# Kernel tuning notes

Measured on AMD Instinct MI355X. Metric: run time of the kernel, lower is better.

Reference implementation:

```python
import jax, jax.numpy as jnp
import numpy as np

B, DIM, H, W = 8, 256, 128, 128
HEADS, D = 8, 32  # num_heads, qkv_dim (key_dim); multi_q_dim = HEADS*D = DIM


def setup_inputs() -> dict:
    key = jax.random.key(0)
    ks = jax.random.split(key, 10)
    def affine(k, n):
        k1, k2 = jax.random.split(k)
        return (1.0 + 0.1 * jax.random.normal(k1, (n,), jnp.float32),
                0.1 * jax.random.normal(k2, (n,), jnp.float32))
    q_scale, q_bias = affine(ks[1], HEADS * D)
    kv_scale, kv_bias = affine(ks[3], D)
    p_scale, p_bias = affine(ks[5], DIM)
    return {
        "input_": jax.random.normal(ks[0], (B, DIM, H, W), jnp.float32),
        "wq": jax.random.normal(ks[6], (HEADS * D, DIM), jnp.float32) / np.sqrt(DIM),
        "q_scale": q_scale, "q_bias": q_bias,
        "wkv": jax.random.normal(ks[7], (D, DIM), jnp.float32) / np.sqrt(DIM),
        "kv_scale": kv_scale, "kv_bias": kv_bias,
        "wp": jax.random.normal(ks[8], (DIM, HEADS * D), jnp.float32) / np.sqrt(HEADS * D),
        "p_scale": p_scale, "p_bias": p_bias,
    }


def conv1x1_bn(x_flat, w, scale, bias):
    # x_flat: [B,C,N]; 1x1 conv (no bias) fused with eval-mode BN affine
    y = jnp.einsum('oc,bcn->bon', w, x_flat)
    return y * scale[:, None] + bias[:, None]


def reference(input_, wq, q_scale, q_bias, wkv, kv_scale, kv_bias, wp, p_scale, p_bias):
    b, c, h, w = input_.shape
    n = h * w
    xf = input_.reshape(b, c, n)
    # queries: [B, heads, D, N]
    q = conv1x1_bn(xf, wq, q_scale, q_bias).reshape(b, HEADS, D, n)
    # shared key/value, one kv head: [B, D, N]
    kv = conv1x1_bn(xf, wkv, kv_scale, kv_bias)
    key_sm = jax.nn.softmax(kv, axis=2)      # softmax over spatial N
    query_sm = jax.nn.softmax(q, axis=2)     # softmax over channel D
    # context = softmax(K) @ V^T : [B, D, D]
    context = jnp.einsum('bdn,ben->bde', key_sm, kv)
    # attended = context^T @ Q (context broadcast over heads): [B, heads, D, N]
    attended = jnp.einsum('bde,bhdn->bhen', context, query_sm)
    av = attended.reshape(b, HEADS * D, n)
    out = conv1x1_bn(jax.nn.relu(av), wp, p_scale, p_bias)
    return out.reshape(b, c, h, w)
```

## Files before the change

### kernel.cpp

```cpp
#include <hip/hip_runtime.h>
#include <hip/hip_bf16.h>

typedef __attribute__((ext_vector_type(8))) short bf16x8;
typedef __attribute__((ext_vector_type(4))) float f32x4;

#define NB 8
#define NC 256
#define ND 32
#define NN 16384
#define TILE_P 32

#define MFMA16(a, b, c) __builtin_amdgcn_mfma_f32_16x16x32_bf16((a), (b), (c), 0, 0, 0)

__device__ __forceinline__ float u2f(unsigned short u) {
  union { unsigned int i; float f; } v; v.i = ((unsigned int)u) << 16; return v.f;
}
__device__ __forceinline__ unsigned short f2u(float f) {
  union { float f; unsigned int i; } v; v.f = f;
  unsigned int x = v.i;
  return (unsigned short)((x + 0x7fffu + ((x >> 16) & 1u)) >> 16);
}
__device__ __forceinline__ float ldg(const void* p, size_t i, int isbf) {
  return isbf ? u2f(((const unsigned short*)p)[i]) : ((const float*)p)[i];
}
__device__ __forceinline__ char* lds_at(char* base, int p, int colb) {
  return base + (p << 9) + (colb ^ ((p & 7) << 4));
}

__global__ __launch_bounds__(256) void detect_kernel(const void* __restrict__ x,
                                                     int* __restrict__ flag) {
  __shared__ int red[4];
  const unsigned int* w = (const unsigned int*)x;
  int cnt = 0;
  for (int i = threadIdx.x; i < 4096; i += 256) {
    unsigned int e = (w[i] >> 7) & 0xFFu;
    cnt += (e >= 100u && e <= 135u) ? 1 : 0;
  }
  for (int off = 32; off; off >>= 1) cnt += __shfl_xor(cnt, off, 64);
  if ((threadIdx.x & 63) == 0) red[threadIdx.x >> 6] = cnt;
  __syncthreads();
  if (threadIdx.x == 0)
    flag[0] = (red[0] + red[1] + red[2] + red[3] > 2048) ? 1 : 0;
}

__global__ __launch_bounds__(256) void prep_weights(
    const void* __restrict__ wq, const void* __restrict__ wp,
    const void* __restrict__ wkv, const int* __restrict__ flag,
    unsigned short* __restrict__ WqPh, unsigned short* __restrict__ WqPl,
    unsigned short* __restrict__ WpPh, unsigned short* __restrict__ WpPl,
    unsigned short* __restrict__ WkPh, unsigned short* __restrict__ WkPl) {
  int isbf = flag[0];
  int idx = blockIdx.x * 256 + threadIdx.x;
  const void* w;
  unsigned short *Ph, *Pl;
  int slot, o, k0;
  if (idx < 16384) {
    int mat = idx >> 13;
    slot = idx & 8191;
    int lane = slot & 63;
    int mbkt = slot >> 6;
    int mb = mbkt & 15, kt = mbkt >> 4;
    o = mb * 16 + (lane & 15);
    k0 = kt * 32 + (lane >> 4) * 8;
    w = mat ? wp : wq;
    Ph = mat ? WpPh : WqPh;
    Pl = mat ? WpPl : WqPl;
  } else {
    slot = idx - 16384;
    int lane = slot & 63;
    int grp = slot >> 6;
    int mb = grp & 1, kt = grp >> 1;
    o = mb * 16 + (lane & 15);
    k0 = kt * 32 + (lane >> 4) * 8;
    w = wkv;
    Ph = WkPh;
    Pl = WkPl;
  }
  unsigned short h[8], lo[8];
#pragma unroll
  for (int e = 0; e < 8; e++) {
    float v = ldg(w, (size_t)o * NC + k0 + e, isbf);
    unsigned short hh = f2u(v);
    h[e] = hh;
    lo[e] = isbf ? (unsigned short)0 : f2u(v - u2f(hh));
  }
  uint4 ph, pl;
  ph.x = h[0] | ((unsigned)h[1] << 16);
  ph.y = h[2] | ((unsigned)h[3] << 16);
  ph.z = h[4] | ((unsigned)h[5] << 16);
  ph.w = h[6] | ((unsigned)h[7] << 16);
  pl.x = lo[0] | ((unsigned)lo[1] << 16);
  pl.y = lo[2] | ((unsigned)lo[3] << 16);
  pl.z = lo[4] | ((unsigned)lo[5] << 16);
  pl.w = lo[6] | ((unsigned)lo[7] << 16);
  *(uint4*)(Ph + (size_t)slot * 8) = ph;
  *(uint4*)(Pl + (size_t)slot * 8) = pl;
}

__global__ __launch_bounds__(256, 4) void kv_ctx(
    const void* __restrict__ x, const unsigned short* __restrict__ WkPh,
    const unsigned short* __restrict__ WkPl, const void* __restrict__ kv_scale,
    const void* __restrict__ kv_bias, const int* __restrict__ flag,
    float* __restrict__ Spart, float* __restrict__ Zpart) {
  __shared__ __align__(16) char pool[32768];
  const int isbf = flag[0];
  const int tid = threadIdx.x;
  const int bid = blockIdx.x;
  const int b = bid >> 9;
  const int n0 = (bid & 511) * 32;
  const int w = tid >> 6, l = tid & 63, g = l >> 4, cc = l & 15;
  const int mi = w >> 1, ni = w & 1;
  const f32x4 zero4 = {0.f, 0.f, 0.f, 0.f};

  {
    const int c0 = (tid >> 3) * 8;
    const int pq = (tid & 7) * 4;
    unsigned short hi[8][4], lo[8][4];
    if (isbf) {
      const unsigned short* xp =
          (const unsigned short*)x + ((size_t)(b * NC + c0)) * NN + n0 + pq;
#pragma unroll
      for (int i = 0; i < 8; i++) {
        ushort4 r = *(const ushort4*)(xp + (size_t)i * NN);
        hi[i][0] = r.x; hi[i][1] = r.y; hi[i][2] = r.z; hi[i][3] = r.w;
      }
    } else {
      const float* xp = (const float*)x + ((size_t)(b * NC + c0)) * NN + n0 + pq;
#pragma unroll
      for (int i = 0; i < 8; i++) {
        float4 v = *(const float4*)(xp + (size_t)i * NN);
        float vv[4] = {v.x, v.y, v.z, v.w};
#pragma unroll
        for (int j = 0; j < 4; j++) {
          unsigned short hh = f2u(vv[j]);
          hi[i][j] = hh;
          lo[i][j] = f2u(vv[j] - u2f(hh));
        }
      }
    }
#pragma unroll
    for (int j = 0; j < 4; j++) {
      int p = pq + j;
      uint4 wv;
      wv.x = hi[0][j] | ((unsigned)hi[1][j] << 16);
      wv.y = hi[2][j] | ((unsigned)hi[3][j] << 16);
      wv.z = hi[4][j] | ((unsigned)hi[5][j] << 16);
      wv.w = hi[6][j] | ((unsigned)hi[7][j] << 16);
      *(uint4*)lds_at(pool, p, c0 * 2) = wv;
      if (!isbf) {
        uint4 wl2;
        wl2.x = lo[0][j] | ((unsigned)lo[1][j] << 16);
        wl2.y = lo[2][j] | ((unsigned)lo[3][j] << 16);
        wl2.z = lo[4][j] | ((unsigned)lo[5][j] << 16);
        wl2.w = lo[6][j] | ((unsigned)lo[7][j] << 16);
        *(uint4*)lds_at(pool + 16384, p, c0 * 2) = wl2;
      }
    }
  }
  __syncthreads();

  f32x4 acc = zero4;
  {
    const bf16x8* Ah = (const bf16x8*)WkPh;
    const bf16x8* Al = (const bf16x8*)WkPl;
#pragma unroll
    for (int kt = 0; kt < 8; kt++) {
      bf16x8 xb = *(const bf16x8*)lds_at(pool, ni * 16 + cc, kt * 64 + 16 * g);
      bf16x8 a = Ah[(kt * 2 + mi) * 64 + l];
      acc = MFMA16(a, xb, acc);
      if (!isbf) {
        bf16x8 xl = *(const bf16x8*)lds_at(pool + 16384, ni * 16 + cc, kt * 64 + 16 * g);
        bf16x8 al = Al[(kt * 2 + mi) * 64 + l];
        acc = MFMA16(a, xl, acc);
        acc = MFMA16(al, xb, acc);
      }
    }
  }

  unsigned short khv[4], klv[4], ehv[4], elv[4];
  float zv[4];
#pragma unroll
  for (int rr = 0; rr < 4; rr++) {
    int d = mi * 16 + 4 * g + rr;
    float v = acc[rr] * ldg(kv_scale, d, isbf) + ldg(kv_bias, d, isbf);
    unsigned short kh = f2u(v);
    khv[rr] = kh;
    klv[rr] = f2u(v - u2f(kh));
    float e = __expf(v);
    zv[rr] = e;
    unsigned short eh = f2u(e);
    ehv[rr] = eh;
    elv[rr] = f2u(e - u2f(eh));
  }
#pragma unroll
  for (int rr = 0; rr < 4; rr++) {
    zv[rr] += __shfl_xor(zv[rr], 1, 64);
    zv[rr] += __shfl_xor(zv[rr], 2, 64);
    zv[rr] += __shfl_xor(zv[rr], 4, 64);
    zv[rr] += __shfl_xor(zv[rr], 8, 64);
  }
  if (cc == 0) {
#pragma unroll
    for (int rr = 0; rr < 4; rr++)
      Zpart[((size_t)bid * 2 + ni) * ND + mi * 16 + 4 * g + rr] = zv[rr];
  }
  __syncthreads();

  {
    char* Eh = pool;
    char* El = pool + 2048;
    char* Kh = pool + 4096;
    char* Kl = pool + 6144;
    int px = ni * 16 + cc;
#pragma unroll
    for (int rr = 0; rr < 4; rr++) {
      int d = mi * 16 + 4 * g + rr;
      int off = d * 64 + ((px * 2) ^ ((d & 3) << 4));
      *(unsigned short*)(Eh + off) = ehv[rr];
      *(unsigned short*)(El + off) = elv[rr];
      *(unsigned short*)(Kh + off) = khv[rr];
      *(unsigned short*)(Kl + off) = klv[rr];
    }
  }
  __syncthreads();

  {
    char* Eh = pool;
    char* El = pool + 2048;
    char* Kh = pool + 4096;
    char* Kl = pool + 6144;
    int ra = mi * 16 + cc;
    int rb = ni * 16 + cc;
    int ca = (16 * g) ^ ((ra & 3) << 4);
    int cb = (16 * g) ^ ((rb & 3) << 4);
    bf16x8 aEh = *(const bf16x8*)(Eh + ra * 64 + ca);
    bf16x8 aEl = *(const bf16x8*)(El + ra * 64 + ca);
    bf16x8 bKh = *(const bf16x8*)(Kh + rb * 64 + cb);
    bf16x8 bKl = *(const bf16x8*)(Kl + rb * 64 + cb);
    f32x4 s = zero4;
    s = MFMA16(aEh, bKh, s);
    s = MFMA16(aEh, bKl, s);
    s = MFMA16(aEl, bKh, s);
    float* sp = Spart + (size_t)bid * 1024;
#pragma unroll
    for (int rr = 0; rr < 4; rr++)
      sp[(mi * 16 + 4 * g + rr) * 32 + ni * 16 + cc] = s[rr];
  }
}

__global__ __launch_bounds__(256) void ctx_redfin(const float* __restrict__ Spart,
                                                  const float* __restrict__ Zpart,
                                                  float* __restrict__ ctx) {
  __shared__ float rs[256], rz[256];
  const int bid = blockIdx.x;
  const int b = bid >> 5, d = bid & 31;
  const int t = threadIdx.x, e = t & 31, j = t >> 5;
  float s = 0.f;
  for (int c = j; c < 512; c += 8)
    s += Spart[((size_t)(b * 512 + c)) * 1024 + d * 32 + e];
  float z = 0.f;
  for (int k = t; k < 1024; k += 256)
    z += Zpart[((size_t)(b * 1024 + k)) * ND + d];
  rs[t] = s; rz[t] = z;
  __syncthreads();
  if (t < 128) { rs[t] += rs[t + 128]; rz[t] += rz[t + 128]; }
  __syncthreads();
  if (t < 64) { rs[t] += rs[t + 64]; rz[t] += rz[t + 64]; }
  __syncthreads();
  if (t < 32) {
    float ss = rs[t] + rs[t + 32];
    float zz = rz[t] + rz[t + 32];
    zz += __shfl_xor(zz, 1, 64);
    zz += __shfl_xor(zz, 2, 64);
    zz += __shfl_xor(zz, 4, 64);
    zz += __shfl_xor(zz, 8, 64);
    zz += __shfl_xor(zz, 16, 64);
    ctx[((size_t)b * ND + d) * ND + t] = ss / zz;
  }
}

#define XT_OFF 0
#define XTL_OFF 16384
#define SMH_OFF 32768
#define SML_OFF 49152
#define YTH_OFF 0
#define YTL_OFF 16384
#define OT_OFF 32768

__global__ __launch_bounds__(256, 2) void fused_main(
    const void* __restrict__ x,
    const unsigned short* __restrict__ WqPh, const unsigned short* __restrict__ WqPl,
    const unsigned short* __restrict__ WpPh, const unsigned short* __restrict__ WpPl,
    const void* __restrict__ q_scale, const void* __restrict__ q_bias,
    const void* __restrict__ p_scale, const void* __restrict__ p_bias,
    const float* __restrict__ ctx, const int* __restrict__ flag,
    void* __restrict__ out) {
  __shared__ __align__(16) char pool[69632];
  __shared__ float qs_l[NC], qb_l[NC], ps_l[NC], pb_l[NC];
  const int isbf = flag[0];
  const int tid = threadIdx.x;
  const int b = blockIdx.x >> 9;
  const int n0 = (blockIdx.x & 511) * TILE_P;
  const int w = tid >> 6;
  const int l = tid & 63;
  const int g = l >> 4;
  const int cc = l & 15;
  const f32x4 zero4 = {0.f, 0.f, 0.f, 0.f};

  qs_l[tid] = ldg(q_scale, tid, isbf);
  qb_l[tid] = ldg(q_bias, tid, isbf);
  ps_l[tid] = ldg(p_scale, tid, isbf);
  pb_l[tid] = ldg(p_bias, tid, isbf);

  bf16x8 cAh[2], cAl[2];
  {
    const float* cb = ctx + (size_t)b * ND * ND;
#pragma unroll
    for (int mp = 0; mp < 2; mp++) {
      bf16x8 ah, al;
#pragma unroll
      for (int el = 0; el < 8; el++) {
        float v = cb[(8 * g + el) * ND + 16 * mp + cc];
        unsigned short hh = f2u(v);
        ah[el] = (short)hh;
        al[el] = (short)f2u(v - u2f(hh));
      }
      cAh[mp] = ah; cAl[mp] = al;
    }
  }

  {
    const int c0 = (tid >> 3) * 8;
    const int pq = (tid & 7) * 4;
    unsigned short hi[8][4], lo[8][4];
    if (isbf) {
      const unsigned short* xp =
          (const unsigned short*)x + ((size_t)(b * NC + c0)) * NN + n0 + pq;
#pragma unroll
      for (int i = 0; i < 8; i++) {
        ushort4 r = *(const ushort4*)(xp + (size_t)i * NN);
        hi[i][0] = r.x; hi[i][1] = r.y; hi[i][2] = r.z; hi[i][3] = r.w;
      }
    } else {
      const float* xp = (const float*)x + ((size_t)(b * NC + c0)) * NN + n0 + pq;
#pragma unroll
      for (int i = 0; i < 8; i++) {
        float4 v = *(const float4*)(xp + (size_t)i * NN);
        float vv[4] = {v.x, v.y, v.z, v.w};
#pragma unroll
        for (int j = 0; j < 4; j++) {
          unsigned short hh = f2u(vv[j]);
          hi[i][j] = hh;
          lo[i][j] = f2u(vv[j] - u2f(hh));
        }
      }
    }
#pragma unroll
    for (int j = 0; j < 4; j++) {
      int p = pq + j;
      uint4 wv;
      wv.x = hi[0][j] | ((unsigned)hi[1][j] << 16);
      wv.y = hi[2][j] | ((unsigned)hi[3][j] << 16);
      wv.z = hi[4][j] | ((unsigned)hi[5][j] << 16);
      wv.w = hi[6][j] | ((unsigned)hi[7][j] << 16);
      *(uint4*)lds_at(pool + XT_OFF, p, c0 * 2) = wv;
      if (!isbf) {
        uint4 wl2;
        wl2.x = lo[0][j] | ((unsigned)lo[1][j] << 16);
        wl2.y = lo[2][j] | ((unsigned)lo[3][j] << 16);
        wl2.z = lo[4][j] | ((unsigned)lo[5][j] << 16);
        wl2.w = lo[6][j] | ((unsigned)lo[7][j] << 16);
        *(uint4*)lds_at(pool + XTL_OFF, p, c0 * 2) = wl2;
      }
    }
  }
  __syncthreads();

  f32x4 acc[4][2];
#pragma unroll
  for (int mi = 0; mi < 4; mi++) { acc[mi][0] = zero4; acc[mi][1] = zero4; }
  {
    const bf16x8* Aq = (const bf16x8*)WqPh;
    const bf16x8* Aql = (const bf16x8*)WqPl;
#pragma unroll
    for (int kt = 0; kt < 8; kt++) {
      bf16x8 xb0 = *(const bf16x8*)lds_at(pool + XT_OFF, cc, kt * 64 + 16 * g);
      bf16x8 xb1 = *(const bf16x8*)lds_at(pool + XT_OFF, 16 + cc, kt * 64 + 16 * g);
      bf16x8 av[4];
#pragma unroll
      for (int mi = 0; mi < 4; mi++) av[mi] = Aq[(kt * 16 + w * 4 + mi) * 64 + l];
#pragma unroll
      for (int mi = 0; mi < 4; mi++) {
        acc[mi][0] = MFMA16(av[mi], xb0, acc[mi][0]);
        acc[mi][1] = MFMA16(av[mi], xb1, acc[mi][1]);
      }
      if (!isbf) {
        bf16x8 xl0 = *(const bf16x8*)lds_at(pool + XTL_OFF, cc, kt * 64 + 16 * g);
        bf16x8 xl1 = *(const bf16x8*)lds_at(pool + XTL_OFF, 16 + cc, kt * 64 + 16 * g);
#pragma unroll
        for (int mi = 0; mi < 4; mi++) {
          bf16x8 al2 = Aql[(kt * 16 + w * 4 + mi) * 64 + l];
          acc[mi][0] = MFMA16(av[mi], xl0, acc[mi][0]);
          acc[mi][1] = MFMA16(av[mi], xl1, acc[mi][1]);
          acc[mi][0] = MFMA16(al2, xb0, acc[mi][0]);
          acc[mi][1] = MFMA16(al2, xb1, acc[mi][1]);
        }
      }
    }
  }

  float inv_s[2][2];
#pragma unroll
  for (int hp = 0; hp < 2; hp++) {
#pragma unroll
    for (int ni = 0; ni < 2; ni++) {
      float e8[8];
      float mx = -3.0e38f;
#pragma unroll
      for (int mi2 = 0; mi2 < 2; mi2++) {
#pragma unroll
        for (int r = 0; r < 4; r++) {
          int o = w * 64 + (2 * hp + mi2) * 16 + 4 * g + r;
          float v = acc[2 * hp + mi2][ni][r] * qs_l[o] + qb_l[o];
          e8[mi2 * 4 + r] = v;
          mx = fmaxf(mx, v);
        }
      }
      mx = fmaxf(mx, __shfl_xor(mx, 16, 64));
      mx = fmaxf(mx, __shfl_xor(mx, 32, 64));
      float s = 0.f;
#pragma unroll
      for (int i2 = 0; i2 < 8; i2++) { e8[i2] = __expf(e8[i2] - mx); s += e8[i2]; }
      s += __shfl_xor(s, 16, 64);
      s += __shfl_xor(s, 32, 64);
      inv_s[hp][ni] = 1.f / s;
      int p = ni * 16 + cc;
#pragma unroll
      for (int mi2 = 0; mi2 < 2; mi2++) {
        int colb = (w * 64 + (2 * hp + mi2) * 16 + 4 * g) * 2;
        unsigned short h[4], lo2[4];
#pragma unroll
        for (int r = 0; r < 4; r++) {
          float ev = e8[mi2 * 4 + r];
          unsigned short hh = f2u(ev);
          h[r] = hh;
          lo2[r] = f2u(ev - u2f(hh));
        }
        uint2 wh, wl2;
        wh.x = h[0] | ((unsigned)h[1] << 16);
        wh.y = h[2] | ((unsigned)h[3] << 16);
        wl2.x = lo2[0] | ((unsigned)lo2[1] << 16);
        wl2.y = lo2[2] | ((unsigned)lo2[3] << 16);
        *(uint2*)lds_at(pool + SMH_OFF, p, colb) = wh;
        *(uint2*)lds_at(pool + SML_OFF, p, colb) = wl2;
      }
    }
  }
  __syncthreads();

#pragma unroll
  for (int hp = 0; hp < 2; hp++) {
    f32x4 cacc[2][2];
#pragma unroll
    for (int mp = 0; mp < 2; mp++) { cacc[mp][0] = zero4; cacc[mp][1] = zero4; }
#pragma unroll
    for (int ni = 0; ni < 2; ni++) {
      int p = ni * 16 + cc;
      int colb = ((2 * w + hp) * 32 + 8 * g) * 2;
      bf16x8 bh = *(const bf16x8*)lds_at(pool + SMH_OFF, p, colb);
      bf16x8 bl = *(const bf16x8*)lds_at(pool + SML_OFF, p, colb);
#pragma unroll
      for (int mp = 0; mp < 2; mp++) {
        cacc[mp][ni] = MFMA16(cAh[mp], bh, cacc[mp][ni]);
        cacc[mp][ni] = MFMA16(cAh[mp], bl, cacc[mp][ni]);
        cacc[mp][ni] = MFMA16(cAl[mp], bh, cacc[mp][ni]);
      }
    }
#pragma unroll
    for (int mp = 0; mp < 2; mp++) {
#pragma unroll
      for (int ni = 0; ni < 2; ni++) {
        int p = ni * 16 + cc;
        float iv = inv_s[hp][ni];
        unsigned short h[4], lo2[4];
#pragma unroll
        for (int r = 0; r < 4; r++) {
          float y = fmaxf(cacc[mp][ni][r] * iv, 0.f);
          unsigned short hh = f2u(y);
          h[r] = hh;
          lo2[r] = f2u(y - u2f(hh));
        }
        int colb = ((2 * w + hp) * 32 + mp * 16 + 4 * g) * 2;
        uint2 wh, wl2;
        wh.x = h[0] | ((unsigned)h[1] << 16);
        wh.y = h[2] | ((unsigned)h[3] << 16);
        wl2.x = lo2[0] | ((unsigned)lo2[1] << 16);
        wl2.y = lo2[2] | ((unsigned)lo2[3] << 16);
        *(uint2*)lds_at(pool + YTH_OFF, p, colb) = wh;
        *(uint2*)lds_at(pool + YTL_OFF, p, colb) = wl2;
      }
    }
  }
  __syncthreads();

  f32x4 oacc[4][2];
#pragma unroll
  for (int mi = 0; mi < 4; mi++) { oacc[mi][0] = zero4; oacc[mi][1] = zero4; }
  {
    const bf16x8* Ap = (const bf16x8*)WpPh;
    const bf16x8* Apl = (const bf16x8*)WpPl;
#pragma unroll
    for (int kt = 0; kt < 8; kt++) {
      bf16x8 yh0 = *(const bf16x8*)lds_at(pool + YTH_OFF, cc, kt * 64 + 16 * g);
      bf16x8 yh1 = *(const bf16x8*)lds_at(pool + YTH_OFF, 16 + cc, kt * 64 + 16 * g);
      bf16x8 yl0 = *(const bf16x8*)lds_at(pool + YTL_OFF, cc, kt * 64 + 16 * g);
      bf16x8 yl1 = *(const bf16x8*)lds_at(pool + YTL_OFF, 16 + cc, kt * 64 + 16 * g);
      bf16x8 av[4];
#pragma unroll
      for (int mi = 0; mi < 4; mi++) av[mi] = Ap[(kt * 16 + w * 4 + mi) * 64 + l];
#pragma unroll
      for (int mi = 0; mi < 4; mi++) {
        oacc[mi][0] = MFMA16(av[mi], yh0, oacc[mi][0]);
        oacc[mi][1] = MFMA16(av[mi], yh1, oacc[mi][1]);
        oacc[mi][0] = MFMA16(av[mi], yl0, oacc[mi][0]);
        oacc[mi][1] = MFMA16(av[mi], yl1, oacc[mi][1]);
      }
      if (!isbf) {
#pragma unroll
        for (int mi = 0; mi < 4; mi++) {
          bf16x8 al2 = Apl[(kt * 16 + w * 4 + mi) * 64 + l];
          oacc[mi][0] = MFMA16(al2, yh0, oacc[mi][0]);
          oacc[mi][1] = MFMA16(al2, yh1, oacc[mi][1]);
        }
      }
    }
  }

  {
    char* OT = pool + OT_OFF;
#pragma unroll
    for (int mi = 0; mi < 4; mi++) {
#pragma unroll
      for (int ni = 0; ni < 2; ni++) {
#pragma unroll
        for (int r = 0; r < 4; r++) {
          int o = w * 64 + mi * 16 + 4 * g + r;
          float v = oacc[mi][ni][r] * ps_l[o] + pb_l[o];
          int p = ni * 16 + cc;
          if (isbf)
            *(unsigned short*)(OT + o * 80 + p * 2) = f2u(v);
          else
            *(float*)(OT + o * 144 + p * 4) = v;
        }
      }
    }
  }
  __syncthreads();
  {
    char* OT = pool + OT_OFF;
    int o = tid;
    size_t gbase = ((size_t)(b * NC + o)) * NN + n0;
    if (isbf) {
      unsigned short* po = (unsigned short*)out + gbase;
#pragma unroll
      for (int k = 0; k < 4; k++)
        *(uint4*)(po + k * 8) = *(const uint4*)(OT + o * 80 + k * 16);
    } else {
      float* po = (float*)out + gbase;
#pragma unroll
      for (int k = 0; k < 8; k++)
        *(float4*)(po + k * 4) = *(const float4*)(OT + o * 144 + k * 16);
    }
  }
}

extern "C" void kernel_launch(void* const* d_in, const int* in_sizes, int n_in,
                              void* d_out, int out_size, void* d_ws, size_t ws_size,
                              hipStream_t stream) {
  const void* input   = d_in[0];
  const void* wq      = d_in[1];
  const void* q_scale = d_in[2];
  const void* q_bias  = d_in[3];
  const void* wkv     = d_in[4];
  const void* kv_scale= d_in[5];
  const void* kv_bias = d_in[6];
  const void* wp      = d_in[7];
  const void* p_scale = d_in[8];
  const void* p_bias  = d_in[9];

  char* w = (char*)d_ws;
  int*  flag = (int*)w;      w += 256;
  float* Spart = (float*)w;  w += (size_t)4096 * 1024 * 4;
  float* Zpart = (float*)w;  w += (size_t)8192 * ND * 4;
  float* ctx  = (float*)w;   w += (size_t)NB * ND * ND * 4;
  unsigned short* WqPh = (unsigned short*)w; w += (size_t)NC * NC * 2;
  unsigned short* WqPl = (unsigned short*)w; w += (size_t)NC * NC * 2;
  unsigned short* WpPh = (unsigned short*)w; w += (size_t)NC * NC * 2;
  unsigned short* WpPl = (unsigned short*)w; w += (size_t)NC * NC * 2;
  unsigned short* WkPh = (unsigned short*)w; w += (size_t)ND * NC * 2;
  unsigned short* WkPl = (unsigned short*)w; w += (size_t)ND * NC * 2;

  detect_kernel<<<1, 256, 0, stream>>>(input, flag);
  prep_weights<<<68, 256, 0, stream>>>(wq, wp, wkv, flag, WqPh, WqPl, WpPh, WpPl,
                                       WkPh, WkPl);
  kv_ctx<<<4096, 256, 0, stream>>>(input, WkPh, WkPl, kv_scale, kv_bias, flag,
                                   Spart, Zpart);
  ctx_redfin<<<256, 256, 0, stream>>>(Spart, Zpart, ctx);
  fused_main<<<4096, 256, 0, stream>>>(input, WqPh, WqPl, WpPh, WpPl,
                                       q_scale, q_bias, p_scale, p_bias,
                                       ctx, flag, (void*)d_out);
}
```

Before: 520.2 us.

## Template kernels on input dtype and coarsen kv_ctx to four tiles per block

Both kv_ctx and fused_main become templates on the bf16 flag, and each is launched twice, with the instance whose type does not match returning early. This lets the compiler drop the dead precision path and size LDS per type, with a smaller pool for bf16 and padded output staging strides. kv_ctx now loops over four 32-pixel tiles per block and accumulates S and Z in registers, cutting partial-sum traffic and the work ctx_redfin must reduce by a factor of four. The cost is two extra empty-grid launches and less parallelism in kv_ctx.

Result: faster. 460.3 us (-11.5%).

```diff
diff --git a/kernel.cpp b/kernel.cpp
--- a/kernel.cpp
+++ b/kernel.cpp
@@ -97,154 +97,168 @@
   *(uint4*)(Pl + (size_t)slot * 8) = pl;
 }
 
+template <int ISBF>
 __global__ __launch_bounds__(256, 4) void kv_ctx(
     const void* __restrict__ x, const unsigned short* __restrict__ WkPh,
     const unsigned short* __restrict__ WkPl, const void* __restrict__ kv_scale,
     const void* __restrict__ kv_bias, const int* __restrict__ flag,
     float* __restrict__ Spart, float* __restrict__ Zpart) {
   __shared__ __align__(16) char pool[32768];
-  const int isbf = flag[0];
+  if (flag[0] != ISBF) return;
   const int tid = threadIdx.x;
   const int bid = blockIdx.x;
-  const int b = bid >> 9;
-  const int n0 = (bid & 511) * 32;
+  const int b = bid >> 7;
+  const int nbase = (bid & 127) * 128;
   const int w = tid >> 6, l = tid & 63, g = l >> 4, cc = l & 15;
   const int mi = w >> 1, ni = w & 1;
   const f32x4 zero4 = {0.f, 0.f, 0.f, 0.f};
-
-  {
-    const int c0 = (tid >> 3) * 8;
-    const int pq = (tid & 7) * 4;
-    unsigned short hi[8][4], lo[8][4];
-    if (isbf) {
-      const unsigned short* xp =
-          (const unsigned short*)x + ((size_t)(b * NC + c0)) * NN + n0 + pq;
-#pragma unroll
-      for (int i = 0; i < 8; i++) {
-        ushort4 r = *(const ushort4*)(xp + (size_t)i * NN);
-        hi[i][0] = r.x; hi[i][1] = r.y; hi[i][2] = r.z; hi[i][3] = r.w;
-      }
-    } else {
-      const float* xp = (const float*)x + ((size_t)(b * NC + c0)) * NN + n0 + pq;
-#pragma unroll
-      for (int i = 0; i < 8; i++) {
-        float4 v = *(const float4*)(xp + (size_t)i * NN);
-        float vv[4] = {v.x, v.y, v.z, v.w};
-#pragma unroll
-        for (int j = 0; j < 4; j++) {
-          unsigned short hh = f2u(vv[j]);
-          hi[i][j] = hh;
-          lo[i][j] = f2u(vv[j] - u2f(hh));
-        }
-      }
-    }
-#pragma unroll
-    for (int j = 0; j < 4; j++) {
-      int p = pq + j;
-      uint4 wv;
-      wv.x = hi[0][j] | ((unsigned)hi[1][j] << 16);
-      wv.y = hi[2][j] | ((unsigned)hi[3][j] << 16);
-      wv.z = hi[4][j] | ((unsigned)hi[5][j] << 16);
-      wv.w = hi[6][j] | ((unsigned)hi[7][j] << 16);
-      *(uint4*)lds_at(pool, p, c0 * 2) = wv;
-      if (!isbf) {
-        uint4 wl2;
-        wl2.x = lo[0][j] | ((unsigned)lo[1][j] << 16);
-        wl2.y = lo[2][j] | ((unsigned)lo[3][j] << 16);
-        wl2.z = lo[4][j] | ((unsigned)lo[5][j] << 16);
-        wl2.w = lo[6][j] | ((unsigned)lo[7][j] << 16);
-        *(uint4*)lds_at(pool + 16384, p, c0 * 2) = wl2;
-      }
-    }
-  }
-  __syncthreads();
-
-  f32x4 acc = zero4;
-  {
-    const bf16x8* Ah = (const bf16x8*)WkPh;
-    const bf16x8* Al = (const bf16x8*)WkPl;
+  const bf16x8* Ah = (const bf16x8*)WkPh;
+  const bf16x8* Al = (const bf16x8*)WkPl;
+
+  float scl[4], bia[4];
+#pragma unroll
+  for (int rr = 0; rr < 4; rr++) {
+    int d = mi * 16 + 4 * g + rr;
+    scl[rr] = ldg(kv_scale, d, ISBF);
+    bia[rr] = ldg(kv_bias, d, ISBF);
+  }
+
+  f32x4 sacc = zero4;
+  float zacc[4] = {0.f, 0.f, 0.f, 0.f};
+
+  for (int st = 0; st < 4; st++) {
+    const int n0 = nbase + st * 32;
+    {
+      const int c0 = (tid >> 3) * 8;
+      const int pq = (tid & 7) * 4;
+      unsigned short hi[8][4], lo[8][4];
+      if (ISBF) {
+        const unsigned short* xp =
+            (const unsigned short*)x + ((size_t)(b * NC + c0)) * NN + n0 + pq;
+#pragma unroll
+        for (int i = 0; i < 8; i++) {
+          ushort4 r = *(const ushort4*)(xp + (size_t)i * NN);
+          hi[i][0] = r.x; hi[i][1] = r.y; hi[i][2] = r.z; hi[i][3] = r.w;
+        }
+      } else {
+        const float* xp = (const float*)x + ((size_t)(b * NC + c0)) * NN + n0 + pq;
+#pragma unroll
+        for (int i = 0; i < 8; i++) {
+          float4 v = *(const float4*)(xp + (size_t)i * NN);
+          float vv[4] = {v.x, v.y, v.z, v.w};
+#pragma unroll
+          for (int j = 0; j < 4; j++) {
+            unsigned short hh = f2u(vv[j]);
+            hi[i][j] = hh;
+            lo[i][j] = f2u(vv[j] - u2f(hh));
+          }
+        }
+      }
+#pragma unroll
+      for (int j = 0; j < 4; j++) {
+        int p = pq + j;
+        uint4 wv;
+        wv.x = hi[0][j] | ((unsigned)hi[1][j] << 16);
+        wv.y = hi[2][j] | ((unsigned)hi[3][j] << 16);
+        wv.z = hi[4][j] | ((unsigned)hi[5][j] << 16);
+        wv.w = hi[6][j] | ((unsigned)hi[7][j] << 16);
+        *(uint4*)lds_at(pool, p, c0 * 2) = wv;
+        if (!ISBF) {
+          uint4 wl2;
+          wl2.x = lo[0][j] | ((unsigned)lo[1][j] << 16);
+          wl2.y = lo[2][j] | ((unsigned)lo[3][j] << 16);
+          wl2.z = lo[4][j] | ((unsigned)lo[5][j] << 16);
+          wl2.w = lo[6][j] | ((unsigned)lo[7][j] << 16);
+          *(uint4*)lds_at(pool + 16384, p, c0 * 2) = wl2;
+        }
+      }
+    }
+    __syncthreads();
+
+    f32x4 acc = zero4;
 #pragma unroll
     for (int kt = 0; kt < 8; kt++) {
       bf16x8 xb = *(const bf16x8*)lds_at(pool, ni * 16 + cc, kt * 64 + 16 * g);
       bf16x8 a = Ah[(kt * 2 + mi) * 64 + l];
       acc = MFMA16(a, xb, acc);
-      if (!isbf) {
+      if (!ISBF) {
         bf16x8 xl = *(const bf16x8*)lds_at(pool + 16384, ni * 16 + cc, kt * 64 + 16 * g);
         bf16x8 al = Al[(kt * 2 + mi) * 64 + l];
         acc = MFMA16(a, xl, acc);
         acc = MFMA16(al, xb, acc);
       }
     }
-  }
-
-  unsigned short khv[4], klv[4], ehv[4], elv[4];
-  float zv[4];
+
+    unsigned short khv[4], klv[4], ehv[4], elv[4];
+#pragma unroll
+    for (int rr = 0; rr < 4; rr++) {
+      float v = acc[rr] * scl[rr] + bia[rr];
+      unsigned short kh = f2u(v);
+      khv[rr] = kh;
+      klv[rr] = f2u(v - u2f(kh));
+      float e = __expf(v);
+      zacc[rr] += e;
+      unsigned short eh = f2u(e);
+      ehv[rr] = eh;
+      elv[rr] = f2u(e - u2f(eh));
+    }
+    __syncthreads();
+
+    {
+      char* Eh = pool;
+      char* El = pool + 2048;
+      char* Kh = pool + 4096;
+      char* Kl = pool + 6144;
+      int px = ni * 16 + cc;
+#pragma unroll
+      for (int rr = 0; rr < 4; rr++) {
+        int d = mi * 16 + 4 * g + rr;
+        int off = d * 64 + ((px * 2) ^ ((d & 3) << 4));
+        *(unsigned short*)(Eh + off) = ehv[rr];
+        *(unsigned short*)(El + off) = elv[rr];
+        *(unsigned short*)(Kh + off) = khv[rr];
+        *(unsigned short*)(Kl + off) = klv[rr];
+      }
+    }
+    __syncthreads();
+
+    {
+      char* Eh = pool;
+      char* El = pool + 2048;
+      char* Kh = pool + 4096;
+      char* Kl = pool + 6144;
+      int ra = mi * 16 + cc;
+      int rb = ni * 16 + cc;
+      int ca = (16 * g) ^ ((ra & 3) << 4);
+      int cb = (16 * g) ^ ((rb & 3) << 4);
+      bf16x8 aEh = *(const bf16x8*)(Eh + ra * 64 + ca);
+      bf16x8 aEl = *(const bf16x8*)(El + ra * 64 + ca);
+      bf16x8 bKh = *(const bf16x8*)(Kh + rb * 64 + cb);
+      bf16x8 bKl = *(const bf16x8*)(Kl + rb * 64 + cb);
+      sacc = MFMA16(aEh, bKh, sacc);
+      sacc = MFMA16(aEh, bKl, sacc);
+      sacc = MFMA16(aEl, bKh, sacc);
+    }
+    __syncthreads();
+  }
+
 #pragma unroll
   for (int rr = 0; rr < 4; rr++) {
-    int d = mi * 16 + 4 * g + rr;
-    float v = acc[rr] * ldg(kv_scale, d, isbf) + ldg(kv_bias, d, isbf);
-    unsigned short kh = f2u(v);
-    khv[rr] = kh;
-    klv[rr] = f2u(v - u2f(kh));
-    float e = __expf(v);
-    zv[rr] = e;
-    unsigned short eh = f2u(e);
-    ehv[rr] = eh;
-    elv[rr] = f2u(e - u2f(eh));
-  }
-#pragma unroll
-  for (int rr = 0; rr < 4; rr++) {
-    zv[rr] += __shfl_xor(zv[rr], 1, 64);
-    zv[rr] += __shfl_xor(zv[rr], 2, 64);
-    zv[rr] += __shfl_xor(zv[rr], 4, 64);
-    zv[rr] += __shfl_xor(zv[rr], 8, 64);
+    zacc[rr] += __shfl_xor(zacc[rr], 1, 64);
+    zacc[rr] += __shfl_xor(zacc[rr], 2, 64);
+    zacc[rr] += __shfl_xor(zacc[rr], 4, 64);
+    zacc[rr] += __shfl_xor(zacc[rr], 8, 64);
   }
   if (cc == 0) {
 #pragma unroll
     for (int rr = 0; rr < 4; rr++)
-      Zpart[((size_t)bid * 2 + ni) * ND + mi * 16 + 4 * g + rr] = zv[rr];
-  }
-  __syncthreads();
-
+      Zpart[((size_t)bid * 2 + ni) * ND + mi * 16 + 4 * g + rr] = zacc[rr];
+  }
   {
-    char* Eh = pool;
-    char* El = pool + 2048;
-    char* Kh = pool + 4096;
-    char* Kl = pool + 6144;
-    int px = ni * 16 + cc;
-#pragma unroll
-    for (int rr = 0; rr < 4; rr++) {
-      int d = mi * 16 + 4 * g + rr;
-      int off = d * 64 + ((px * 2) ^ ((d & 3) << 4));
-      *(unsigned short*)(Eh + off) = ehv[rr];
-      *(unsigned short*)(El + off) = elv[rr];
-      *(unsigned short*)(Kh + off) = khv[rr];
-      *(unsigned short*)(Kl + off) = klv[rr];
-    }
-  }
-  __syncthreads();
-
-  {
-    char* Eh = pool;
-    char* El = pool + 2048;
-    char* Kh = pool + 4096;
-    char* Kl = pool + 6144;
-    int ra = mi * 16 + cc;
-    int rb = ni * 16 + cc;
-    int ca = (16 * g) ^ ((ra & 3) << 4);
-    int cb = (16 * g) ^ ((rb & 3) << 4);
-    bf16x8 aEh = *(const bf16x8*)(Eh + ra * 64 + ca);
-    bf16x8 aEl = *(const bf16x8*)(El + ra * 64 + ca);
-    bf16x8 bKh = *(const bf16x8*)(Kh + rb * 64 + cb);
-    bf16x8 bKl = *(const bf16x8*)(Kl + rb * 64 + cb);
-    f32x4 s = zero4;
-    s = MFMA16(aEh, bKh, s);
-    s = MFMA16(aEh, bKl, s);
-    s = MFMA16(aEl, bKh, s);
     float* sp = Spart + (size_t)bid * 1024;
 #pragma unroll
     for (int rr = 0; rr < 4; rr++)
-      sp[(mi * 16 + 4 * g + rr) * 32 + ni * 16 + cc] = s[rr];
+      sp[(mi * 16 + 4 * g + rr) * 32 + ni * 16 + cc] = sacc[rr];
   }
 }
 
@@ -256,11 +270,9 @@
   const int b = bid >> 5, d = bid & 31;
   const int t = threadIdx.x, e = t & 31, j = t >> 5;
   float s = 0.f;
-  for (int c = j; c < 512; c += 8)
-    s += Spart[((size_t)(b * 512 + c)) * 1024 + d * 32 + e];
-  float z = 0.f;
-  for (int k = t; k < 1024; k += 256)
-    z += Zpart[((size_t)(b * 1024 + k)) * ND + d];
+  for (int c = j; c < 128; c += 8)
+    s += Spart[((size_t)(b * 128 + c)) * 1024 + d * 32 + e];
+  float z = Zpart[((size_t)(b * 256 + t)) * ND + d];
   rs[t] = s; rz[t] = z;
   __syncthreads();
   if (t < 128) { rs[t] += rs[t + 128]; rz[t] += rz[t + 128]; }
@@ -279,14 +291,7 @@
   }
 }
 
-#define XT_OFF 0
-#define XTL_OFF 16384
-#define SMH_OFF 32768
-#define SML_OFF 49152
-#define YTH_OFF 0
-#define YTL_OFF 16384
-#define OT_OFF 32768
-
+template <int ISBF>
 __global__ __launch_bounds__(256, 2) void fused_main(
     const void* __restrict__ x,
     const unsigned short* __restrict__ WqPh, const unsigned short* __restrict__ WqPl,
@@ -295,9 +300,18 @@
     const void* __restrict__ p_scale, const void* __restrict__ p_bias,
     const float* __restrict__ ctx, const int* __restrict__ flag,
     void* __restrict__ out) {
-  __shared__ __align__(16) char pool[69632];
+  constexpr int XT_O = 0;
+  constexpr int XTL_O = 16384;
+  constexpr int SMH_O = ISBF ? 16384 : 32768;
+  constexpr int SML_O = ISBF ? 32768 : 49152;
+  constexpr int YTH_O = 0;
+  constexpr int YTL_O = 16384;
+  constexpr int OT_O = ISBF ? 16384 : 32768;
+  constexpr int OT_STR = ISBF ? 88 : 132;
+  constexpr int POOL = ISBF ? 49152 : 69632;
+  __shared__ __align__(16) char pool[POOL];
   __shared__ float qs_l[NC], qb_l[NC], ps_l[NC], pb_l[NC];
-  const int isbf = flag[0];
+  if (flag[0] != ISBF) return;
   const int tid = threadIdx.x;
   const int b = blockIdx.x >> 9;
   const int n0 = (blockIdx.x & 511) * TILE_P;
@@ -307,10 +321,10 @@
   const int cc = l & 15;
   const f32x4 zero4 = {0.f, 0.f, 0.f, 0.f};
 
-  qs_l[tid] = ldg(q_scale, tid, isbf);
-  qb_l[tid] = ldg(q_bias, tid, isbf);
-  ps_l[tid] = ldg(p_scale, tid, isbf);
-  pb_l[tid] = ldg(p_bias, tid, isbf);
+  qs_l[tid] = ldg(q_scale, tid, ISBF);
+  qb_l[tid] = ldg(q_bias, tid, ISBF);
+  ps_l[tid] = ldg(p_scale, tid, ISBF);
+  pb_l[tid] = ldg(p_bias, tid, ISBF);
 
   bf16x8 cAh[2], cAl[2];
   {
@@ -333,7 +347,7 @@
     const int c0 = (tid >> 3) * 8;
     const int pq = (tid & 7) * 4;
     unsigned short hi[8][4], lo[8][4];
-    if (isbf) {
+    if (ISBF) {
       const unsigned short* xp =
           (const unsigned short*)x + ((size_t)(b * NC + c0)) * NN + n0 + pq;
 #pragma unroll
@@ -363,14 +377,14 @@
       wv.y = hi[2][j] | ((unsigned)hi[3][j] << 16);
       wv.z = hi[4][j] | ((unsigned)hi[5][j] << 16);
       wv.w = hi[6][j] | ((unsigned)hi[7][j] << 16);
-      *(uint4*)lds_at(pool + XT_OFF, p, c0 * 2) = wv;
-      if (!isbf) {
+      *(uint4*)lds_at(pool + XT_O, p, c0 * 2) = wv;
+      if (!ISBF) {
         uint4 wl2;
         wl2.x = lo[0][j] | ((unsigned)lo[1][j] << 16);
         wl2.y = lo[2][j] | ((unsigned)lo[3][j] << 16);
         wl2.z = lo[4][j] | ((unsigned)lo[5][j] << 16);
         wl2.w = lo[6][j] | ((unsigned)lo[7][j] << 16);
-        *(uint4*)lds_at(pool + XTL_OFF, p, c0 * 2) = wl2;
+        *(uint4*)lds_at(pool + XTL_O, p, c0 * 2) = wl2;
       }
     }
   }
@@ -384,8 +398,8 @@
     const bf16x8* Aql = (const bf16x8*)WqPl;
 #pragma unroll
     for (int kt = 0; kt < 8; kt++) {
-      bf16x8 xb0 = *(const bf16x8*)lds_at(pool + XT_OFF, cc, kt * 64 + 16 * g);
-      bf16x8 xb1 = *(const bf16x8*)lds_at(pool + XT_OFF, 16 + cc, kt * 64 + 16 * g);
+      bf16x8 xb0 = *(const bf16x8*)lds_at(pool + XT_O, cc, kt * 64 + 16 * g);
+      bf16x8 xb1 = *(const bf16x8*)lds_at(pool + XT_O, 16 + cc, kt * 64 + 16 * g);
       bf16x8 av[4];
 #pragma unroll
       for (int mi = 0; mi < 4; mi++) av[mi] = Aq[(kt * 16 + w * 4 + mi) * 64 + l];
@@ -394,9 +408,9 @@
         acc[mi][0] = MFMA16(av[mi], xb0, acc[mi][0]);
         acc[mi][1] = MFMA16(av[mi], xb1, acc[mi][1]);
       }
-      if (!isbf) {
-        bf16x8 xl0 = *(const bf16x8*)lds_at(pool + XTL_OFF, cc, kt * 64 + 16 * g);
-        bf16x8 xl1 = *(const bf16x8*)lds_at(pool + XTL_OFF, 16 + cc, kt * 64 + 16 * g);
+      if (!ISBF) {
+        bf16x8 xl0 = *(const bf16x8*)lds_at(pool + XTL_O, cc, kt * 64 + 16 * g);
+        bf16x8 xl1 = *(const bf16x8*)lds_at(pool + XTL_O, 16 + cc, kt * 64 + 16 * g);
 #pragma unroll
         for (int mi = 0; mi < 4; mi++) {
           bf16x8 al2 = Aql[(kt * 16 + w * 4 + mi) * 64 + l];
@@ -451,8 +465,8 @@
         wh.y = h[2] | ((unsigned)h[3] << 16);
         wl2.x = lo2[0] | ((unsigned)lo2[1] << 16);
         wl2.y = lo2[2] | ((unsigned)lo2[3] << 16);
-        *(uint2*)lds_at(pool + SMH_OFF, p, colb) = wh;
-        *(uint2*)lds_at(pool + SML_OFF, p, colb) = wl2;
+        *(uint2*)lds_at(pool + SMH_O, p, colb) = wh;
+        *(uint2*)lds_at(pool + SML_O, p, colb) = wl2;
       }
     }
   }
@@ -467,8 +481,8 @@
     for (int ni = 0; ni < 2; ni++) {
       int p = ni * 16 + cc;
       int colb = ((2 * w + hp) * 32 + 8 * g) * 2;
-      bf16x8 bh = *(const bf16x8*)lds_at(pool + SMH_OFF, p, colb);
-      bf16x8 bl = *(const bf16x8*)lds_at(pool + SML_OFF, p, colb);
+      bf16x8 bh = *(const bf16x8*)lds_at(pool + SMH_O, p, colb);
+      bf16x8 bl = *(const bf16x8*)lds_at(pool + SML_O, p, colb);
 #pragma unroll
       for (int mp = 0; mp < 2; mp++) {
         cacc[mp][ni] = MFMA16(cAh[mp], bh, cacc[mp][ni]);
@@ -491,13 +505,14 @@
           lo2[r] = f2u(y - u2f(hh));
         }
         int colb = ((2 * w + hp) * 32 + mp * 16 + 4 * g) * 2;
-        uint2 wh, wl2;
+        uint2 wh;
         wh.x = h[0] | ((unsigned)h[1] << 16);
         wh.y = h[2] | ((unsigned)h[3] << 16);
+        *(uint2*)lds_at(pool + YTH_O, p, colb) = wh;
+        uint2 wl2;
         wl2.x = lo2[0] | ((unsigned)lo2[1] << 16);
         wl2.y = lo2[2] | ((unsigned)lo2[3] << 16);
-        *(uint2*)lds_at(pool + YTH_OFF, p, colb) = wh;
-        *(uint2*)lds_at(pool + YTL_OFF, p, colb) = wl2;
+        *(uint2*)lds_at(pool + YTL_O, p, colb) = wl2;
       }
     }
   }
@@ -511,10 +526,10 @@
     const bf16x8* Apl = (const bf16x8*)WpPl;
 #pragma unroll
     for (int kt = 0; kt < 8; kt++) {
-      bf16x8 yh0 = *(const bf16x8*)lds_at(pool + YTH_OFF, cc, kt * 64 + 16 * g);
-      bf16x8 yh1 = *(const bf16x8*)lds_at(pool + YTH_OFF, 16 + cc, kt * 64 + 16 * g);
-      bf16x8 yl0 = *(const bf16x8*)lds_at(pool + YTL_OFF, cc, kt * 64 + 16 * g);
-      bf16x8 yl1 = *(const bf16x8*)lds_at(pool + YTL_OFF, 16 + cc, kt * 64 + 16 * g);
+      bf16x8 yh0 = *(const bf16x8*)lds_at(pool + YTH_O, cc, kt * 64 + 16 * g);
+      bf16x8 yh1 = *(const bf16x8*)lds_at(pool + YTH_O, 16 + cc, kt * 64 + 16 * g);
+      bf16x8 yl0 = *(const bf16x8*)lds_at(pool + YTL_O, cc, kt * 64 + 16 * g);
+      bf16x8 yl1 = *(const bf16x8*)lds_at(pool + YTL_O, 16 + cc, kt * 64 + 16 * g);
       bf16x8 av[4];
 #pragma unroll
       for (int mi = 0; mi < 4; mi++) av[mi] = Ap[(kt * 16 + w * 4 + mi) * 64 + l];
@@ -525,7 +540,7 @@
         oacc[mi][0] = MFMA16(av[mi], yl0, oacc[mi][0]);
         oacc[mi][1] = MFMA16(av[mi], yl1, oacc[mi][1]);
       }
-      if (!isbf) {
+      if (!ISBF) {
 #pragma unroll
         for (int mi = 0; mi < 4; mi++) {
           bf16x8 al2 = Apl[(kt * 16 + w * 4 + mi) * 64 + l];
@@ -537,7 +552,7 @@
   }
 
   {
-    char* OT = pool + OT_OFF;
+    char* OT = pool + OT_O;
 #pragma unroll
     for (int mi = 0; mi < 4; mi++) {
 #pragma unroll
@@ -547,29 +562,38 @@
           int o = w * 64 + mi * 16 + 4 * g + r;
           float v = oacc[mi][ni][r] * ps_l[o] + pb_l[o];
           int p = ni * 16 + cc;
-          if (isbf)
-            *(unsigned short*)(OT + o * 80 + p * 2) = f2u(v);
+          if (ISBF)
+            *(unsigned short*)(OT + o * OT_STR + p * 2) = f2u(v);
           else
-            *(float*)(OT + o * 144 + p * 4) = v;
+            *(float*)(OT + o * OT_STR + p * 4) = v;
         }
       }
     }
   }
   __syncthreads();
   {
-    char* OT = pool + OT_OFF;
+    char* OT = pool + OT_O;
     int o = tid;
     size_t gbase = ((size_t)(b * NC + o)) * NN + n0;
-    if (isbf) {
+    if (ISBF) {
       unsigned short* po = (unsigned short*)out + gbase;
 #pragma unroll
-      for (int k = 0; k < 4; k++)
-        *(uint4*)(po + k * 8) = *(const uint4*)(OT + o * 80 + k * 16);
+      for (int k = 0; k < 4; k++) {
+        uint2 a = *(const uint2*)(OT + o * OT_STR + k * 16);
+        uint2 b2 = *(const uint2*)(OT + o * OT_STR + k * 16 + 8);
+        *(uint4*)(po + k * 8) = make_uint4(a.x, a.y, b2.x, b2.y);
+      }
     } else {
       float* po = (float*)out + gbase;
 #pragma unroll
-      for (int k = 0; k < 8; k++)
-        *(float4*)(po + k * 4) = *(const float4*)(OT + o * 144 + k * 16);
+      for (int k = 0; k < 8; k++) {
+        float4 v;
+        v.x = *(const float*)(OT + o * OT_STR + (k * 4 + 0) * 4);
+        v.y = *(const float*)(OT + o * OT_STR + (k * 4 + 1) * 4);
+        v.z = *(const float*)(OT + o * OT_STR + (k * 4 + 2) * 4);
+        v.w = *(const float*)(OT + o * OT_STR + (k * 4 + 3) * 4);
+        *(float4*)(po + k * 4) = v;
+      }
     }
   }
 }
@@ -590,8 +614,8 @@
 
   char* w = (char*)d_ws;
   int*  flag = (int*)w;      w += 256;
-  float* Spart = (float*)w;  w += (size_t)4096 * 1024 * 4;
-  float* Zpart = (float*)w;  w += (size_t)8192 * ND * 4;
+  float* Spart = (float*)w;  w += (size_t)1024 * 1024 * 4;
+  float* Zpart = (float*)w;  w += (size_t)2048 * ND * 4;
   float* ctx  = (float*)w;   w += (size_t)NB * ND * ND * 4;
   unsigned short* WqPh = (unsigned short*)w; w += (size_t)NC * NC * 2;
   unsigned short* WqPl = (unsigned short*)w; w += (size_t)NC * NC * 2;
@@ -603,10 +627,15 @@
   detect_kernel<<<1, 256, 0, stream>>>(input, flag);
   prep_weights<<<68, 256, 0, stream>>>(wq, wp, wkv, flag, WqPh, WqPl, WpPh, WpPl,
                                        WkPh, WkPl);
-  kv_ctx<<<4096, 256, 0, stream>>>(input, WkPh, WkPl, kv_scale, kv_bias, flag,
-                                   Spart, Zpart);
+  kv_ctx<1><<<1024, 256, 0, stream>>>(input, WkPh, WkPl, kv_scale, kv_bias, flag,
+                                      Spart, Zpart);
+  kv_ctx<0><<<1024, 256, 0, stream>>>(input, WkPh, WkPl, kv_scale, kv_bias, flag,
+                                      Spart, Zpart);
   ctx_redfin<<<256, 256, 0, stream>>>(Spart, Zpart, ctx);
-  fused_main<<<4096, 256, 0, stream>>>(input, WqPh, WqPl, WpPh, WpPl,
-                                       q_scale, q_bias, p_scale, p_bias,
-                                       ctx, flag, (void*)d_out);
-}
+  fused_main<1><<<4096, 256, 0, stream>>>(input, WqPh, WqPl, WpPh, WpPl,
+                                          q_scale, q_bias, p_scale, p_bias,
+                                          ctx, flag, (void*)d_out);
+  fused_main<0><<<4096, 256, 0, stream>>>(input, WqPh, WqPl, WpPh, WpPl,
+                                          q_scale, q_bias, p_scale, p_bias,
+                                          ctx, flag, (void*)d_out);
+}
```
